# Kernel optimization log

Measured on AMD Instinct MI355X. Metric: run time of the kernel, lower is better.

## Reference

```python
import jax, jax.numpy as jnp
import numpy as np

N, M, E, HID, H = 50000, 4000, 320000, 128, 2
EPS = 1e-5  # torch BatchNorm1d eps


def _lrelu(x):
    return jnp.where(x >= 0, x, 0.2 * x)


def _bn(x, g, b):
    # BatchNorm1d in training mode: biased batch statistics over dim 0
    m = x.mean(0)
    v = ((x - m) ** 2).mean(0)
    return g * (x - m) * jax.lax.rsqrt(v + EPS) + b


def _seg_softmax(a, idx, n):
    # softmax of a[E,heads] normalized per node index idx (PyG softmax)
    mx = jax.ops.segment_max(a, idx, num_segments=n)
    e = jnp.exp(a - mx[idx])
    s = jax.ops.segment_sum(e, idx, num_segments=n)
    return e / s[idx]


def _hgconv(x, he_n, he_e, he_w, W, att, bias, heads):
    # PyG HypergraphConv(use_attention=True, concat=False)
    xl = (x @ W).reshape(N, heads, HID)                  # lin(x) -> [N,heads,C]
    # hyperedge_attr = incidence^T @ x  (matches to_dense_adj path in HGAT)
    ea = jax.ops.segment_sum(x[he_n], he_e, num_segments=M)  # [M,F]
    eal = (ea @ W).reshape(M, heads, HID)                # lin(hyperedge_attr)
    a = (jnp.concatenate([xl[he_n], eal[he_e]], axis=-1) * att[0]).sum(-1)  # [E,heads]
    a = _seg_softmax(_lrelu(a), he_n, N)
    # degree normalizations
    Dn = jax.ops.segment_sum(he_w[he_e], he_n, num_segments=N)
    Dinv = jnp.where(Dn > 0, 1.0 / Dn, 0.0)
    Bn = jax.ops.segment_sum(jnp.ones((E,), x.dtype), he_e, num_segments=M)
    Binv = jnp.where(Bn > 0, 1.0 / Bn, 0.0)
    # node -> hyperedge
    m1 = Binv[he_e][:, None, None] * xl[he_n] * a[..., None]
    eo = jax.ops.segment_sum(m1, he_e, num_segments=M)   # [M,heads,C]
    # hyperedge -> node
    m2 = Dinv[he_n][:, None, None] * eo[he_e] * a[..., None]
    out = jax.ops.segment_sum(m2, he_n, num_segments=N)  # [N,heads,C]
    return out.mean(1) + bias                            # concat=False -> head mean


def _forward(x, he_w, lin1_w, lin1_b, bn1_g, bn1_b, h1_w, h1_att, h1_b,
             bn2_g, bn2_b, h2_w, h2_att, h2_b, bn3_g, bn3_b,
             lin2_w, lin2_b, bn4_g, bn4_b, he_n, he_e):
    src = x
    x = _bn(_lrelu(x @ lin1_w + lin1_b), bn1_g, bn1_b)
    x2 = _hgconv(x, he_n, he_e, he_w, h1_w, h1_att, h1_b, H)
    x = _bn(x + x2, bn2_g, bn2_b)
    x2 = _hgconv(x, he_n, he_e, he_w, h2_w, h2_att, h2_b, 1)
    x = _bn(x + x2, bn3_g, bn3_b)
    x = _lrelu(x @ lin2_w + lin2_b)
    return _bn(src + x, bn4_g, bn4_b)


def setup_inputs() -> dict:
    key = jax.random.key(0)
    ks = jax.random.split(key, 10)
    s = 0.05
    he_n = jax.random.randint(ks[0], (E,), 0, N, dtype=jnp.int32)
    he_e = (jnp.arange(E, dtype=jnp.int32) % M)  # every hyperedge id used
    return {
        'x': jax.random.normal(ks[1], (N, 128), jnp.float32),
        'he_n': he_n, 'he_e': he_e,
        'he_w': jnp.ones((M,), jnp.float32),
        'lin1_w': jax.random.normal(ks[2], (128, HID), jnp.float32) * s,
        'lin1_b': jnp.zeros((HID,), jnp.float32),
        'bn1_g': jnp.ones((HID,), jnp.float32), 'bn1_b': jnp.zeros((HID,), jnp.float32),
        'h1_w': jax.random.normal(ks[3], (HID, H * HID), jnp.float32) * s,
        'h1_att': jax.random.normal(ks[4], (1, H, 2 * HID), jnp.float32) * s,
        'h1_b': jnp.zeros((HID,), jnp.float32),
        'bn2_g': jnp.ones((HID,), jnp.float32), 'bn2_b': jnp.zeros((HID,), jnp.float32),
        'h2_w': jax.random.normal(ks[5], (HID, HID), jnp.float32) * s,
        'h2_att': jax.random.normal(ks[6], (1, 1, 2 * HID), jnp.float32) * s,
        'h2_b': jnp.zeros((HID,), jnp.float32),
        'bn3_g': jnp.ones((HID,), jnp.float32), 'bn3_b': jnp.zeros((HID,), jnp.float32),
        'lin2_w': jax.random.normal(ks[7], (HID, 128), jnp.float32) * s,
        'lin2_b': jnp.zeros((128,), jnp.float32),
        'bn4_g': jnp.ones((128,), jnp.float32), 'bn4_b': jnp.zeros((128,), jnp.float32),
    }


def reference(x, he_n, he_e, he_w, lin1_w, lin1_b, bn1_g, bn1_b, h1_w, h1_att, h1_b,
              bn2_g, bn2_b, h2_w, h2_att, h2_b, bn3_g, bn3_b,
              lin2_w, lin2_b, bn4_g, bn4_b):
    return _forward(x, he_w, lin1_w, lin1_b, bn1_g, bn1_b, h1_w, h1_att, h1_b,
                    bn2_g, bn2_b, h2_w, h2_att, h2_b, bn3_g, bn3_b,
                    lin2_w, lin2_b, bn4_g, bn4_b, he_n, he_e)
```

## Files before the change

### kernel.cpp

```cpp
#include <hip/hip_runtime.h>
#include <math.h>

constexpr int Nn = 50000;
constexpr int Mm = 4000;
constexpr int Ee = 320000;
constexpr int KPB = Ee / Mm;
constexpr float BINV = 1.0f / (float)KPB;
constexpr float EPSf = 1e-5f;
constexpr int NBKT = 16;
constexpr int NBSCAN = 49;

__device__ __forceinline__ float lrelu_f(float x) { return x >= 0.f ? x : 0.2f * x; }

__device__ __forceinline__ float wave_sum(float v) {
#pragma unroll
    for (int o = 32; o >= 1; o >>= 1) v += __shfl_xor(v, o, 64);
    return v;
}

__device__ __forceinline__ void finalize_to_lds(const float* __restrict__ st,
                                                const float* __restrict__ g,
                                                const float* __restrict__ b,
                                                float* ABsh, int t) {
    if (t < 128) {
        double ds = 0, dq = 0;
#pragma unroll
        for (int i = 0; i < NBKT; i++) {
            ds += (double)st[i * 256 + t];
            dq += (double)st[i * 256 + 128 + t];
        }
        double mean = ds / (double)Nn;
        double var = dq / (double)Nn - mean * mean;
        float rstd = (float)(1.0 / sqrt(var + (double)EPSf));
        float A = g[t] * rstd;
        ABsh[t] = A;
        ABsh[128 + t] = b[t] - (float)mean * A;
    }
    __syncthreads();
}

__device__ void scan_body(const int* __restrict__ counts, int* __restrict__ offs,
                          int b, int t) {
    __shared__ int sdi[256];
    int pre = 0;
    for (int i = t; i < b * 1024; i += 256) pre += counts[i];
    sdi[t] = pre;
    __syncthreads();
    for (int st = 128; st >= 1; st >>= 1) {
        if (t < st) sdi[t] += sdi[t + st];
        __syncthreads();
    }
    int run0 = sdi[0];
    __syncthreads();
    int c4[4];
    int s = 0;
#pragma unroll
    for (int i = 0; i < 4; i++) {
        int n = b * 1024 + t * 4 + i;
        c4[i] = (n < Nn) ? counts[n] : 0;
        s += c4[i];
    }
    sdi[t] = s;
    __syncthreads();
    for (int off = 1; off < 256; off <<= 1) {
        int v = (t >= off) ? sdi[t - off] : 0;
        __syncthreads();
        sdi[t] += v;
        __syncthreads();
    }
    int run = sdi[t] - s + run0;
#pragma unroll
    for (int i = 0; i < 4; i++) {
        int n = b * 1024 + t * 4 + i;
        if (n < Nn) offs[n] = run;
        run += c4[i];
    }
    if (b == NBSCAN - 1 && t == 255) offs[Nn] = run0 + sdi[255];
}

template <int ROWS, bool LRELU, bool PROBN, bool RESID, bool STATS, bool PACKH2, bool SCANX>
__global__ __launch_bounds__(256) void gemmT(const float* __restrict__ A, size_t aystride,
                                             const float* __restrict__ B, int ldb,
                                             const float* __restrict__ bias, float scale,
                                             const float* __restrict__ stIn,
                                             const float* __restrict__ fing,
                                             const float* __restrict__ finb,
                                             const float* __restrict__ resid,
                                             float* __restrict__ stF,
                                             float* __restrict__ C, int ldc, int R,
                                             int gemmBlocksX,
                                             const int* __restrict__ counts,
                                             int* __restrict__ offs) {
    constexpr int RPT = ROWS / 16;
    const int t = threadIdx.x;
    if (SCANX && (int)blockIdx.x >= gemmBlocksX) {
        if (blockIdx.y == 0) scan_body(counts, offs, blockIdx.x - gemmBlocksX, t);
        return;
    }
    __shared__ float As[16][ROWS + 4];
    __shared__ float Bs[16][128];
    __shared__ float Sred[STATS ? 16 : 1][STATS ? 128 : 1];
    __shared__ float ABsh[PROBN ? 256 : 1];
    const int ty = t >> 4, tx = t & 15;
    const int row0 = blockIdx.x * ROWS;
    const int bcol = blockIdx.y * 128;
    A += (size_t)blockIdx.y * aystride;

    if (PROBN) finalize_to_lds(stIn, fing, finb, ABsh, t);

    float4 acc[RPT][2];
#pragma unroll
    for (int i = 0; i < RPT; i++)
#pragma unroll
        for (int q = 0; q < 2; q++) acc[i][q] = make_float4(0.f, 0.f, 0.f, 0.f);

    for (int k0 = 0; k0 < 128; k0 += 16) {
        {
            int r = t >> 3, kc = (t & 7) * 2;
            int rr = row0 + r;
            rr = rr < R ? rr : R - 1;
            float2 av = *(const float2*)(A + (size_t)rr * 128 + k0 + kc);
            if (PROBN) {
                av.x = av.x * ABsh[k0 + kc] + ABsh[128 + k0 + kc];
                av.y = av.y * ABsh[k0 + kc + 1] + ABsh[128 + k0 + kc + 1];
            }
            As[kc + 0][r] = av.x;
            As[kc + 1][r] = av.y;
        }
        {
            int kk = t >> 5, c4 = (t & 31) * 4;
            float4 bv0 = *(const float4*)(B + (size_t)(k0 + kk) * ldb + bcol + c4);
            float4 bv1 = *(const float4*)(B + (size_t)(k0 + kk + 8) * ldb + bcol + c4);
            *(float4*)&Bs[kk][c4] = bv0;
            *(float4*)&Bs[kk + 8][c4] = bv1;
        }
        __syncthreads();
#pragma unroll
        for (int kk = 0; kk < 16; kk++) {
            float ar[RPT];
            float2 a2 = *(const float2*)&As[kk][ty * 2];
            ar[0] = a2.x; ar[RPT - 1] = a2.y;
            float4 b0 = *(const float4*)&Bs[kk][4 * tx];
            float4 b1 = *(const float4*)&Bs[kk][64 + 4 * tx];
#pragma unroll
            for (int i = 0; i < RPT; i++) {
                acc[i][0].x = fmaf(ar[i], b0.x, acc[i][0].x);
                acc[i][0].y = fmaf(ar[i], b0.y, acc[i][0].y);
                acc[i][0].z = fmaf(ar[i], b0.z, acc[i][0].z);
                acc[i][0].w = fmaf(ar[i], b0.w, acc[i][0].w);
                acc[i][1].x = fmaf(ar[i], b1.x, acc[i][1].x);
                acc[i][1].y = fmaf(ar[i], b1.y, acc[i][1].y);
                acc[i][1].z = fmaf(ar[i], b1.z, acc[i][1].z);
                acc[i][1].w = fmaf(ar[i], b1.w, acc[i][1].w);
            }
        }
        __syncthreads();
    }

    float4 bv0 = make_float4(0.f, 0.f, 0.f, 0.f), bv1 = bv0;
    if (bias) {
        bv0 = *(const float4*)(bias + bcol + 4 * tx);
        bv1 = *(const float4*)(bias + bcol + 64 + 4 * tx);
    }
    float4 cs0 = make_float4(0.f, 0.f, 0.f, 0.f), cs1 = cs0, cq0 = cs0, cq1 = cs0;
#pragma unroll
    for (int i = 0; i < RPT; i++) {
        int row = row0 + ty * RPT + i;
        if (row >= R) continue;
        float4 v0, v1;
        v0.x = acc[i][0].x * scale + bv0.x; v0.y = acc[i][0].y * scale + bv0.y;
        v0.z = acc[i][0].z * scale + bv0.z; v0.w = acc[i][0].w * scale + bv0.w;
        v1.x = acc[i][1].x * scale + bv1.x; v1.y = acc[i][1].y * scale + bv1.y;
        v1.z = acc[i][1].z * scale + bv1.z; v1.w = acc[i][1].w * scale + bv1.w;
        if (LRELU) {
            v0.x = lrelu_f(v0.x); v0.y = lrelu_f(v0.y); v0.z = lrelu_f(v0.z); v0.w = lrelu_f(v0.w);
            v1.x = lrelu_f(v1.x); v1.y = lrelu_f(v1.y); v1.z = lrelu_f(v1.z); v1.w = lrelu_f(v1.w);
        }
        if (RESID) {
            float4 r0 = *(const float4*)(resid + (size_t)row * 128 + bcol + 4 * tx);
            float4 r1 = *(const float4*)(resid + (size_t)row * 128 + bcol + 64 + 4 * tx);
            v0.x += r0.x; v0.y += r0.y; v0.z += r0.z; v0.w += r0.w;
            v1.x += r1.x; v1.y += r1.y; v1.z += r1.z; v1.w += r1.w;
        }
        if (PACKH2) {
            int h = blockIdx.y;
            float* c0 = C + (size_t)row * ldc + 8 * tx + 2 * h;
            *(float2*)(c0) = make_float2(v0.x, v0.y);
            *(float2*)(c0 + 4) = make_float2(v0.z, v0.w);
            float* c1 = C + (size_t)row * ldc + 128 + 8 * tx + 2 * h;
            *(float2*)(c1) = make_float2(v1.x, v1.y);
            *(float2*)(c1 + 4) = make_float2(v1.z, v1.w);
        } else {
            *(float4*)(C + (size_t)row * ldc + bcol + 4 * tx) = v0;
            *(float4*)(C + (size_t)row * ldc + bcol + 64 + 4 * tx) = v1;
        }
        if (STATS) {
            cs0.x += v0.x; cs0.y += v0.y; cs0.z += v0.z; cs0.w += v0.w;
            cs1.x += v1.x; cs1.y += v1.y; cs1.z += v1.z; cs1.w += v1.w;
            cq0.x += v0.x * v0.x; cq0.y += v0.y * v0.y; cq0.z += v0.z * v0.z; cq0.w += v0.w * v0.w;
            cq1.x += v1.x * v1.x; cq1.y += v1.y * v1.y; cq1.z += v1.z * v1.z; cq1.w += v1.w * v1.w;
        }
    }
    if (STATS) {
        int bkt = blockIdx.x & (NBKT - 1);
#pragma unroll
        for (int pass = 0; pass < 2; pass++) {
            *(float4*)&Sred[ty][4 * tx] = pass ? cq0 : cs0;
            *(float4*)&Sred[ty][64 + 4 * tx] = pass ? cq1 : cs1;
            __syncthreads();
            if (t < 128) {
                float tot = 0.f;
#pragma unroll
                for (int r = 0; r < 16; r++) tot += Sred[r][t];
                atomicAdd(&stF[bkt * 256 + pass * 128 + t], tot);
            }
            __syncthreads();
        }
    }
}

__global__ void count_edges_watt(const int* __restrict__ he_n, int* __restrict__ counts,
                                 const float* __restrict__ h1_w, const float* __restrict__ h1_att,
                                 const float* __restrict__ h2_w, const float* __restrict__ h2_att,
                                 float* __restrict__ wnA, float* __restrict__ weA) {
    int t = threadIdx.x;
    if (blockIdx.x == 1250) {
        for (int j = 0; j < 3; j++) {
            int id = t + 256 * j;
            if (id >= 768) break;
            int which = id / 384;
            int rem = id % 384;
            int h3 = rem >> 7, k = rem & 127;
            float s = 0.f;
            if (h3 < 2) {
                const float* wrow = h1_w + (size_t)k * 256 + h3 * 128;
                const float* arow = h1_att + h3 * 256 + which * 128;
                for (int c = 0; c < 128; c++) s += wrow[c] * arow[c];
            } else {
                const float* wrow = h2_w + (size_t)k * 128;
                const float* arow = h2_att + which * 128;
                for (int c = 0; c < 128; c++) s += wrow[c] * arow[c];
            }
            (which ? weA : wnA)[h3 * 128 + k] = s;
        }
        return;
    }
    int e = blockIdx.x * 256 + t;
    if (e < Ee) atomicAdd(&counts[he_n[e]], 1);
}

template <int H, bool FILL>
__global__ __launch_bounds__(256) void bn_dots(const float* __restrict__ X,
                                               const float* __restrict__ stIn,
                                               const float* __restrict__ fing,
                                               const float* __restrict__ finb,
                                               float* __restrict__ ABout,
                                               const float* __restrict__ wn,
                                               const float* __restrict__ we,
                                               float* __restrict__ an,
                                               float* __restrict__ pe,
                                               const int* __restrict__ he_n,
                                               const int* __restrict__ offs,
                                               int* __restrict__ cursor,
                                               int* __restrict__ eid, int mainBlocks) {
    int t = threadIdx.x;
    if (FILL && (int)blockIdx.x >= mainBlocks) {
        int e = (blockIdx.x - mainBlocks) * 256 + t;
        if (e < Ee) {
            int n = he_n[e];
            int p = atomicAdd(&cursor[n], 1);
            eid[offs[n] + p] = e;
        }
        return;
    }
    __shared__ float ABsh[256];
    finalize_to_lds(stIn, fing, finb, ABsh, t);
    if (blockIdx.x == 0) ABout[t] = ABsh[t];
    int w = t >> 6, lane = t & 63;
    float a0 = ABsh[lane], a1 = ABsh[lane + 64];
    float b0 = ABsh[128 + lane], b1 = ABsh[192 + lane];
    float wn0[H], wn1[H], we0[H], we1[H];
#pragma unroll
    for (int h = 0; h < H; h++) {
        wn0[h] = wn[h * 128 + lane]; wn1[h] = wn[h * 128 + 64 + lane];
        we0[h] = we[h * 128 + lane]; we1[h] = we[h * 128 + 64 + lane];
    }
#pragma unroll
    for (int nn = 0; nn < 4; nn++) {
        int row = blockIdx.x * 16 + w * 4 + nn;
        const float* xr = X + (size_t)row * 128;
        float v0 = xr[lane] * a0 + b0;
        float v1 = xr[lane + 64] * a1 + b1;
        float pv[H], qv[H];
#pragma unroll
        for (int h = 0; h < H; h++) {
            pv[h] = wave_sum(v0 * wn0[h] + v1 * wn1[h]);
            qv[h] = wave_sum(v0 * we0[h] + v1 * we1[h]);
        }
        if (lane == 0) {
            if (H == 2) {
                *(float2*)&an[row * 2] = make_float2(pv[0], pv[1]);
                *(float2*)&pe[row * 2] = make_float2(qv[0], qv[1]);
            } else {
                an[row] = pv[0];
                pe[row] = qv[0];
            }
        }
    }
}

__global__ __launch_bounds__(256) void bn_out(const float* __restrict__ X,
                                              const float* __restrict__ stIn,
                                              const float* __restrict__ fing,
                                              const float* __restrict__ finb,
                                              float* __restrict__ Y) {
    __shared__ float ABsh[256];
    int t = threadIdx.x;
    finalize_to_lds(stIn, fing, finb, ABsh, t);
    int w = t >> 6, lane = t & 63;
    float a0 = ABsh[lane], a1 = ABsh[lane + 64];
    float b0 = ABsh[128 + lane], b1 = ABsh[192 + lane];
#pragma unroll
    for (int nn = 0; nn < 4; nn++) {
        int row = blockIdx.x * 16 + w * 4 + nn;
        const float* xr = X + (size_t)row * 128;
        float* yr = Y + (size_t)row * 128;
        yr[lane] = xr[lane] * a0 + b0;
        yr[lane + 64] = xr[lane + 64] * a1 + b1;
    }
}

template <int H>
__global__ __launch_bounds__(256) void ea_from_pe(const int* __restrict__ he_n,
                                                  const float* __restrict__ pe,
                                                  float* __restrict__ ae) {
    int w = threadIdx.x >> 6, lane = threadIdx.x & 63;
    int m = blockIdx.x * 4 + w;
    if (m >= Mm) return;
    float s[H];
#pragma unroll
    for (int h = 0; h < H; h++) s[h] = 0.f;
    for (int k = lane; k < KPB; k += 64) {
        int idx = he_n[m + k * Mm];
        if (H == 2) {
            float2 p2 = *(const float2*)(pe + (size_t)idx * 2);
            s[0] += p2.x;
            s[H - 1] += p2.y;
        } else {
            s[0] += pe[idx];
        }
    }
#pragma unroll
    for (int h = 0; h < H; h++) s[h] = wave_sum(s[h]);
    if (lane == 0)
#pragma unroll
        for (int h = 0; h < H; h++) ae[m * H + h] = s[h];
}

template <int H>
__global__ __launch_bounds__(256) void seg_softmax(const int* __restrict__ offs,
                                                   const int* __restrict__ eid,
                                                   const float* __restrict__ an,
                                                   const float* __restrict__ ae,
                                                   const float* __restrict__ he_w,
                                                   float* __restrict__ aw,
                                                   float* __restrict__ sdl) {
    int t = threadIdx.x;
    int wv = t >> 6, lane = t & 63;
    int q = lane >> 3, li = lane & 7;
    int n = blockIdx.x * 32 + wv * 8 + q;
    bool valid = n < Nn;
    int base = valid ? offs[n] : 0;
    int deg = valid ? offs[n + 1] - base : 0;
    float anv[H];
#pragma unroll
    for (int h = 0; h < H; h++) anv[h] = valid ? an[n * H + h] : 0.f;

    bool h0 = li < deg, h1 = li + 8 < deg;
    int e0 = 0, e1 = 0, m0 = 0, m1 = 0;
    float l0[H], l1[H];
    float mx[H];
#pragma unroll
    for (int h = 0; h < H; h++) { mx[h] = -INFINITY; l0[h] = 0.f; l1[h] = 0.f; }
    if (h0) {
        e0 = eid[base + li];
        m0 = e0 % Mm;
#pragma unroll
        for (int h = 0; h < H; h++) {
            l0[h] = lrelu_f(anv[h] + ae[m0 * H + h]);
            mx[h] = fmaxf(mx[h], l0[h]);
        }
    }
    if (h1) {
        e1 = eid[base + li + 8];
        m1 = e1 % Mm;
#pragma unroll
        for (int h = 0; h < H; h++) {
            l1[h] = lrelu_f(anv[h] + ae[m1 * H + h]);
            mx[h] = fmaxf(mx[h], l1[h]);
        }
    }
    for (int c = li + 16; c < deg; c += 8) {
        int e = eid[base + c];
        int m = e % Mm;
#pragma unroll
        for (int h = 0; h < H; h++) mx[h] = fmaxf(mx[h], lrelu_f(anv[h] + ae[m * H + h]));
    }
#pragma unroll
    for (int h = 0; h < H; h++) {
#pragma unroll
        for (int o = 1; o <= 4; o <<= 1) mx[h] = fmaxf(mx[h], __shfl_xor(mx[h], o, 64));
    }
    float sm[H], p0[H], p1[H];
#pragma unroll
    for (int h = 0; h < H; h++) { sm[h] = 0.f; p0[h] = 0.f; p1[h] = 0.f; }
    float dn = 0.f;
    if (h0) {
        dn += he_w[m0];
#pragma unroll
        for (int h = 0; h < H; h++) { p0[h] = expf(l0[h] - mx[h]); sm[h] += p0[h]; }
    }
    if (h1) {
        dn += he_w[m1];
#pragma unroll
        for (int h = 0; h < H; h++) { p1[h] = expf(l1[h] - mx[h]); sm[h] += p1[h]; }
    }
    for (int c = li + 16; c < deg; c += 8) {
        int e = eid[base + c];
        int m = e % Mm;
        dn += he_w[m];
#pragma unroll
        for (int h = 0; h < H; h++) sm[h] += expf(lrelu_f(anv[h] + ae[m * H + h]) - mx[h]);
    }
#pragma unroll
    for (int o = 1; o <= 4; o <<= 1) dn += __shfl_xor(dn, o, 64);
#pragma unroll
    for (int h = 0; h < H; h++) {
#pragma unroll
        for (int o = 1; o <= 4; o <<= 1) sm[h] += __shfl_xor(sm[h], o, 64);
    }
    float Dv = dn > 0.f ? 1.0f / dn : 0.0f;
    float premul = Dv * (H == 2 ? 0.5f : 1.0f);
    if (h0) {
        float p[H];
#pragma unroll
        for (int h = 0; h < H; h++) p[h] = p0[h] / sm[h];
        if (H == 2) {
            *(float2*)(aw + (size_t)e0 * 2) = make_float2(p[0], p[1]);
            *(float4*)(sdl + (size_t)(base + li) * 4) =
                make_float4(__int_as_float(m0), p[0] * premul, p[H - 1] * premul, 0.f);
        } else {
            aw[e0] = p[0];
            *(float2*)(sdl + (size_t)(base + li) * 2) = make_float2(__int_as_float(m0), p[0] * premul);
        }
    }
    if (h1) {
        float p[H];
#pragma unroll
        for (int h = 0; h < H; h++) p[h] = p1[h] / sm[h];
        if (H == 2) {
            *(float2*)(aw + (size_t)e1 * 2) = make_float2(p[0], p[1]);
            *(float4*)(sdl + (size_t)(base + li + 8) * 4) =
                make_float4(__int_as_float(m1), p[0] * premul, p[H - 1] * premul, 0.f);
        } else {
            aw[e1] = p[0];
            *(float2*)(sdl + (size_t)(base + li + 8) * 2) =
                make_float2(__int_as_float(m1), p[0] * premul);
        }
    }
    for (int c = li + 16; c < deg; c += 8) {
        int e = eid[base + c];
        int m = e % Mm;
        float p[H];
#pragma unroll
        for (int h = 0; h < H; h++) p[h] = expf(lrelu_f(anv[h] + ae[m * H + h]) - mx[h]) / sm[h];
        if (H == 2) {
            *(float2*)(aw + (size_t)e * 2) = make_float2(p[0], p[1]);
            *(float4*)(sdl + (size_t)(base + c) * 4) =
                make_float4(__int_as_float(m), p[0] * premul, p[H - 1] * premul, 0.f);
        } else {
            aw[e] = p[0];
            *(float2*)(sdl + (size_t)(base + c) * 2) = make_float2(__int_as_float(m), p[0] * premul);
        }
    }
}

template <int H>
__global__ __launch_bounds__(256) void s_build(const float* __restrict__ X,
                                               const float* __restrict__ AB,
                                               const int* __restrict__ he_n,
                                               const float* __restrict__ aw,
                                               float* __restrict__ S) {
    __shared__ int idx[KPB];
    __shared__ float av[KPB][H];
    __shared__ float red[8][H][128];
    int m = blockIdx.x, t = threadIdx.x;
    int g = t >> 5, l = t & 31;
    if (t < KPB) idx[t] = he_n[m + t * Mm];
    for (int q2 = t; q2 < KPB * H; q2 += 256) {
        int k = q2 / H, h = q2 - k * H;
        av[k][h] = aw[(size_t)(m + k * Mm) * H + h];
    }
    __syncthreads();
    float4 A4 = ((const float4*)AB)[l];
    float4 B4 = ((const float4*)(AB + 128))[l];
    float4 acc[H];
#pragma unroll
    for (int h = 0; h < H; h++) acc[h] = make_float4(0.f, 0.f, 0.f, 0.f);
#pragma unroll
    for (int kk = 0; kk < KPB / 8; kk++) {
        int k = g + kk * 8;
        float4 v = ((const float4*)(X + (size_t)idx[k] * 128))[l];
        v.x = v.x * A4.x + B4.x;
        v.y = v.y * A4.y + B4.y;
        v.z = v.z * A4.z + B4.z;
        v.w = v.w * A4.w + B4.w;
#pragma unroll
        for (int h = 0; h < H; h++) {
            float a = av[k][h];
            acc[h].x = fmaf(a, v.x, acc[h].x);
            acc[h].y = fmaf(a, v.y, acc[h].y);
            acc[h].z = fmaf(a, v.z, acc[h].z);
            acc[h].w = fmaf(a, v.w, acc[h].w);
        }
    }
#pragma unroll
    for (int h = 0; h < H; h++) *(float4*)&red[g][h][l * 4] = acc[h];
    __syncthreads();
    if (t < 32 * H) {
        int h = t >> 5, l2 = t & 31;
        float4 s = make_float4(0.f, 0.f, 0.f, 0.f);
#pragma unroll
        for (int gg = 0; gg < 8; gg++) {
            float4 r = *(const float4*)&red[gg][h][l2 * 4];
            s.x += r.x; s.y += r.y; s.z += r.z; s.w += r.w;
        }
        ((float4*)(S + ((size_t)h * Mm + m) * 128))[l2] = s;
    }
}

template <int H>
__global__ __launch_bounds__(256) void node_agg(const int* __restrict__ offs,
                                                const float* __restrict__ sdl,
                                                const float* __restrict__ eo,
                                                const float* __restrict__ bias,
                                                const float* __restrict__ AB,
                                                float* __restrict__ stF,
                                                float* __restrict__ T) {
    __shared__ float smem[4][256];
    __shared__ float redS[4][128], redQ[4][128];
    int t = threadIdx.x;
    int w = t >> 6, lane = t & 63;
    int n0 = blockIdx.x * 16 + w * 4;
    int o = offs[n0 + (lane < 4 ? lane : 4)];
    int b0 = __shfl(o, 0, 64);
    int b1 = __shfl(o, 1, 64);
    int b2 = __shfl(o, 2, 64);
    int b3 = __shfl(o, 3, 64);
    int b4 = __shfl(o, 4, 64);
    int cnt = b4 - b0;
    int cnt64 = cnt < 64 ? cnt : 64;

    if (lane < cnt64) {
        int slot = b0 + lane;
        if (H == 2) {
            *(float4*)&smem[w][4 * lane] = *(const float4*)(sdl + (size_t)slot * 4);
        } else {
            *(float2*)&smem[w][2 * lane] = *(const float2*)(sdl + (size_t)slot * 2);
        }
    }
    __syncthreads();

    int s1 = min(b1 - b0, cnt64), s2 = min(b2 - b0, cnt64), s3 = min(b3 - b0, cnt64);
    float2 acc0 = make_float2(0.f, 0.f), acc1 = acc0, acc2 = acc0, acc3 = acc0;

#define NA_BODY(ACC, CBEG, CEND)                                                \
    {                                                                           \
        int c = (CBEG);                                                         \
        for (; c + 1 < (CEND); c += 2) {                                        \
            if (H == 2) {                                                       \
                float4 sa = *(const float4*)&smem[w][4 * c];                    \
                float4 sb = *(const float4*)&smem[w][4 * (c + 1)];              \
                float4 ea = *(const float4*)(eo + (size_t)__float_as_int(sa.x) * 256 + 4 * lane); \
                float4 eb = *(const float4*)(eo + (size_t)__float_as_int(sb.x) * 256 + 4 * lane); \
                ACC.x += sa.y * ea.x + sa.z * ea.z + sb.y * eb.x + sb.z * eb.z; \
                ACC.y += sa.y * ea.y + sa.z * ea.w + sb.y * eb.y + sb.z * eb.w; \
            } else {                                                            \
                float2 sa = *(const float2*)&smem[w][2 * c];                    \
                float2 sb = *(const float2*)&smem[w][2 * (c + 1)];              \
                float2 ea = *(const float2*)(eo + (size_t)__float_as_int(sa.x) * 128 + 2 * lane); \
                float2 eb = *(const float2*)(eo + (size_t)__float_as_int(sb.x) * 128 + 2 * lane); \
                ACC.x += sa.y * ea.x + sb.y * eb.x;                             \
                ACC.y += sa.y * ea.y + sb.y * eb.y;                             \
            }                                                                   \
        }                                                                       \
        if (c < (CEND)) {                                                       \
            if (H == 2) {                                                       \
                float4 sa = *(const float4*)&smem[w][4 * c];                    \
                float4 ea = *(const float4*)(eo + (size_t)__float_as_int(sa.x) * 256 + 4 * lane); \
                ACC.x += sa.y * ea.x + sa.z * ea.z;                             \
                ACC.y += sa.y * ea.y + sa.z * ea.w;                             \
            } else {                                                            \
                float2 sa = *(const float2*)&smem[w][2 * c];                    \
                float2 ea = *(const float2*)(eo + (size_t)__float_as_int(sa.x) * 128 + 2 * lane); \
                ACC.x += sa.y * ea.x;                                           \
                ACC.y += sa.y * ea.y;                                           \
            }                                                                   \
        }                                                                       \
    }
    NA_BODY(acc0, 0, s1)
    NA_BODY(acc1, s1, s2)
    NA_BODY(acc2, s2, s3)
    NA_BODY(acc3, s3, cnt64)
#undef NA_BODY

    for (int ss = 64; ss < cnt; ss++) {
        int slot = b0 + ss;
        int j = (slot >= b1) + (slot >= b2) + (slot >= b3);
        float cx, cy;
        if (H == 2) {
            float4 v = *(const float4*)(sdl + (size_t)slot * 4);
            float4 ev = *(const float4*)(eo + (size_t)__float_as_int(v.x) * 256 + 4 * lane);
            cx = v.y * ev.x + v.z * ev.z;
            cy = v.y * ev.y + v.z * ev.w;
        } else {
            float2 v = *(const float2*)(sdl + (size_t)slot * 2);
            float2 ev = *(const float2*)(eo + (size_t)__float_as_int(v.x) * 128 + 2 * lane);
            cx = v.y * ev.x;
            cy = v.y * ev.y;
        }
        if (j == 0) { acc0.x += cx; acc0.y += cy; }
        else if (j == 1) { acc1.x += cx; acc1.y += cy; }
        else if (j == 2) { acc2.x += cx; acc2.y += cy; }
        else { acc3.x += cx; acc3.y += cy; }
    }

    int col = 2 * lane;
    float2 A2 = *(const float2*)(AB + col);
    float2 B2 = *(const float2*)(AB + 128 + col);
    float2 bi = *(const float2*)(bias + col);
    float cs0 = 0.f, cs1 = 0.f, cq0 = 0.f, cq1 = 0.f;
    float2 accs[4] = {acc0, acc1, acc2, acc3};
#pragma unroll
    for (int j = 0; j < 4; j++) {
        int n = n0 + j;
        float2 xr = *(const float2*)(T + (size_t)n * 128 + col);
        float r0 = xr.x * A2.x + B2.x + bi.x + accs[j].x;
        float r1 = xr.y * A2.y + B2.y + bi.y + accs[j].y;
        *(float2*)(T + (size_t)n * 128 + col) = make_float2(r0, r1);
        cs0 += r0; cs1 += r1;
        cq0 += r0 * r0; cq1 += r1 * r1;
    }
    redS[w][col] = cs0; redS[w][col + 1] = cs1;
    redQ[w][col] = cq0; redQ[w][col + 1] = cq1;
    __syncthreads();
    if (t < 128) {
        float s = 0.f, qq = 0.f;
#pragma unroll
        for (int ww = 0; ww < 4; ww++) { s += redS[ww][t]; qq += redQ[ww][t]; }
        int bkt = blockIdx.x & (NBKT - 1);
        atomicAdd(&stF[bkt * 256 + t], s);
        atomicAdd(&stF[bkt * 256 + 128 + t], qq);
    }
}

extern "C" void kernel_launch(void* const* d_in, const int* in_sizes, int n_in,
                              void* d_out, int out_size, void* d_ws, size_t ws_size,
                              hipStream_t stream) {
    const float* x = (const float*)d_in[0];
    const int* he_n = (const int*)d_in[1];
    const float* he_w = (const float*)d_in[3];
    const float* lin1_w = (const float*)d_in[4];
    const float* lin1_b = (const float*)d_in[5];
    const float* bn1_g = (const float*)d_in[6];
    const float* bn1_b = (const float*)d_in[7];
    const float* h1_w = (const float*)d_in[8];
    const float* h1_att = (const float*)d_in[9];
    const float* h1_b = (const float*)d_in[10];
    const float* bn2_g = (const float*)d_in[11];
    const float* bn2_b = (const float*)d_in[12];
    const float* h2_w = (const float*)d_in[13];
    const float* h2_att = (const float*)d_in[14];
    const float* h2_b = (const float*)d_in[15];
    const float* bn3_g = (const float*)d_in[16];
    const float* bn3_b = (const float*)d_in[17];
    const float* lin2_w = (const float*)d_in[18];
    const float* lin2_b = (const float*)d_in[19];
    const float* bn4_g = (const float*)d_in[20];
    const float* bn4_b = (const float*)d_in[21];
    float* out = (float*)d_out;

    char* ws = (char*)d_ws;
    size_t off = 0;
    auto alloc = [&](size_t bytes) -> char* {
        char* p = ws + off;
        off = (off + bytes + 255) & ~(size_t)255;
        return p;
    };
    int* counts = (int*)alloc((size_t)Nn * 4);
    int* cursor = (int*)alloc((size_t)Nn * 4);
    float* stats = (float*)alloc((size_t)4 * NBKT * 256 * 4);
    size_t zbytes = off;
    int* offs = (int*)alloc((size_t)(Nn + 1) * 4);
    int* eid = (int*)alloc((size_t)Ee * 4);
    float* an = (float*)alloc((size_t)Nn * 2 * 4);
    float* pe = (float*)alloc((size_t)Nn * 2 * 4);
    float* ae = (float*)alloc((size_t)Mm * 2 * 4);
    float* aw = (float*)alloc((size_t)Ee * 2 * 4);
    float* sdl = (float*)alloc((size_t)Ee * 4 * 4);
    float* S = (float*)alloc((size_t)2 * Mm * 128 * 4);
    float* eo = (float*)alloc((size_t)2 * Mm * 128 * 4);
    float* wnA = (float*)alloc(384 * 4);
    float* weA = (float*)alloc(384 * 4);
    float* AB = (float*)alloc(2 * 256 * 4);
    float* buf = (float*)alloc((size_t)Nn * 128 * 4);

    float* st0 = stats;
    float* st1 = stats + NBKT * 256;
    float* st2 = stats + 2 * NBKT * 256;
    float* st3 = stats + 3 * NBKT * 256;
    float *AB1 = AB, *AB2 = AB + 256;

    hipMemsetAsync(d_ws, 0, zbytes, stream);

    constexpr int GB32 = (Nn + 31) / 32;
    count_edges_watt<<<1251, 256, 0, stream>>>(he_n, counts, h1_w, h1_att, h2_w, h2_att,
                                               wnA, weA);

    gemmT<32, true, false, false, true, false, true><<<dim3(GB32 + NBSCAN, 1), 256, 0, stream>>>(
        x, 0, lin1_w, 128, lin1_b, 1.f, nullptr, nullptr, nullptr, nullptr, st0, buf, 128, Nn,
        GB32, counts, offs);
    bn_dots<2, true><<<3125 + 1250, 256, 0, stream>>>(buf, st0, bn1_g, bn1_b, AB1, wnA, weA,
                                                      an, pe, he_n, offs, cursor, eid, 3125);

    ea_from_pe<2><<<Mm / 4, 256, 0, stream>>>(he_n, pe, ae);
    seg_softmax<2><<<(Nn + 31) / 32, 256, 0, stream>>>(offs, eid, an, ae, he_w, aw, sdl);
    s_build<2><<<Mm, 256, 0, stream>>>(buf, AB1, he_n, aw, S);
    gemmT<32, false, false, false, false, true, false><<<dim3(125, 2), 256, 0, stream>>>(
        S, (size_t)Mm * 128, h1_w, 256, nullptr, BINV, nullptr, nullptr, nullptr, nullptr,
        nullptr, eo, 256, Mm, 125, nullptr, nullptr);
    node_agg<2><<<3125, 256, 0, stream>>>(offs, sdl, eo, h1_b, AB1, st1, buf);

    bn_dots<1, false><<<3125, 256, 0, stream>>>(buf, st1, bn2_g, bn2_b, AB2, wnA + 256,
                                                weA + 256, an, pe, nullptr, nullptr, nullptr,
                                                nullptr, 3125);

    ea_from_pe<1><<<Mm / 4, 256, 0, stream>>>(he_n, pe, ae);
    seg_softmax<1><<<(Nn + 31) / 32, 256, 0, stream>>>(offs, eid, an, ae, he_w, aw, sdl);
    s_build<1><<<Mm, 256, 0, stream>>>(buf, AB2, he_n, aw, S);
    gemmT<32, false, false, false, false, false, false><<<dim3(125, 1), 256, 0, stream>>>(
        S, 0, h2_w, 128, nullptr, BINV, nullptr, nullptr, nullptr, nullptr, nullptr,
        eo, 128, Mm, 125, nullptr, nullptr);
    node_agg<1><<<3125, 256, 0, stream>>>(offs, sdl, eo, h2_b, AB2, st2, buf);

    gemmT<32, true, true, true, true, false, false><<<dim3(GB32, 1), 256, 0, stream>>>(
        buf, 0, lin2_w, 128, lin2_b, 1.f, st2, bn3_g, bn3_b, x, st3, buf, 128, Nn,
        GB32, nullptr, nullptr);
    bn_out<<<3125, 256, 0, stream>>>(buf, st3, bn4_g, bn4_b, out);
}
```

Baseline: 404.5 us.

## Shift preprocessing stages one launch later to drop the separate count kernel

The edge-count and attention-weight precompute blocks now ride along with the first GEMM launch, the prefix scan moves into the first bn_dots launch, and the CSR fill moves into the first ea_from_pe launch. The standalone count kernel is removed, saving one launch and its serialization point. Each dependent stage still runs after its producer because kernels on the stream are ordered. In exchange, the extra side blocks lengthen the tail of the kernels that host them, and the preprocessing chain now spans three launches.

```diff
diff --git a/kernel.cpp b/kernel.cpp
--- a/kernel.cpp
+++ b/kernel.cpp
@@ -9,6 +9,8 @@
 constexpr float EPSf = 1e-5f;
 constexpr int NBKT = 16;
 constexpr int NBSCAN = 49;
+constexpr int NBFILL = 1250;
+constexpr int NBCNT = 1251;
 
 __device__ __forceinline__ float lrelu_f(float x) { return x >= 0.f ? x : 0.2f * x; }
 
@@ -78,7 +80,30 @@
     if (b == NBSCAN - 1 && t == 255) offs[Nn] = run0 + sdi[255];
 }
 
-template <int ROWS, bool LRELU, bool PROBN, bool RESID, bool STATS, bool PACKH2, bool SCANX>
+__device__ void watt_body(const float* __restrict__ h1_w, const float* __restrict__ h1_att,
+                          const float* __restrict__ h2_w, const float* __restrict__ h2_att,
+                          float* __restrict__ wnA, float* __restrict__ weA, int t) {
+    for (int j = 0; j < 3; j++) {
+        int id = t + 256 * j;
+        if (id >= 768) break;
+        int which = id / 384;
+        int rem = id % 384;
+        int h3 = rem >> 7, k = rem & 127;
+        float s = 0.f;
+        if (h3 < 2) {
+            const float* wrow = h1_w + (size_t)k * 256 + h3 * 128;
+            const float* arow = h1_att + h3 * 256 + which * 128;
+            for (int c = 0; c < 128; c++) s += wrow[c] * arow[c];
+        } else {
+            const float* wrow = h2_w + (size_t)k * 128;
+            const float* arow = h2_att + which * 128;
+            for (int c = 0; c < 128; c++) s += wrow[c] * arow[c];
+        }
+        (which ? weA : wnA)[h3 * 128 + k] = s;
+    }
+}
+
+template <int ROWS, bool LRELU, bool PROBN, bool RESID, bool STATS, bool PACKH2, bool CNTW>
 __global__ __launch_bounds__(256) void gemmT(const float* __restrict__ A, size_t aystride,
                                              const float* __restrict__ B, int ldb,
                                              const float* __restrict__ bias, float scale,
@@ -89,12 +114,24 @@
                                              float* __restrict__ stF,
                                              float* __restrict__ C, int ldc, int R,
                                              int gemmBlocksX,
-                                             const int* __restrict__ counts,
-                                             int* __restrict__ offs) {
+                                             const int* __restrict__ he_n,
+                                             int* __restrict__ counts,
+                                             const float* __restrict__ h1_w,
+                                             const float* __restrict__ h1_att,
+                                             const float* __restrict__ h2_w,
+                                             const float* __restrict__ h2_att,
+                                             float* __restrict__ wnA,
+                                             float* __restrict__ weA) {
     constexpr int RPT = ROWS / 16;
     const int t = threadIdx.x;
-    if (SCANX && (int)blockIdx.x >= gemmBlocksX) {
-        if (blockIdx.y == 0) scan_body(counts, offs, blockIdx.x - gemmBlocksX, t);
+    if (CNTW && (int)blockIdx.x >= gemmBlocksX) {
+        int cb = blockIdx.x - gemmBlocksX;
+        if (cb < NBCNT - 1) {
+            int e = cb * 256 + t;
+            if (e < Ee) atomicAdd(&counts[he_n[e]], 1);
+        } else {
+            watt_body(h1_w, h1_att, h2_w, h2_att, wnA, weA, t);
+        }
         return;
     }
     __shared__ float As[16][ROWS + 4];
@@ -219,37 +256,7 @@
     }
 }
 
-__global__ void count_edges_watt(const int* __restrict__ he_n, int* __restrict__ counts,
-                                 const float* __restrict__ h1_w, const float* __restrict__ h1_att,
-                                 const float* __restrict__ h2_w, const float* __restrict__ h2_att,
-                                 float* __restrict__ wnA, float* __restrict__ weA) {
-    int t = threadIdx.x;
-    if (blockIdx.x == 1250) {
-        for (int j = 0; j < 3; j++) {
-            int id = t + 256 * j;
-            if (id >= 768) break;
-            int which = id / 384;
-            int rem = id % 384;
-            int h3 = rem >> 7, k = rem & 127;
-            float s = 0.f;
-            if (h3 < 2) {
-                const float* wrow = h1_w + (size_t)k * 256 + h3 * 128;
-                const float* arow = h1_att + h3 * 256 + which * 128;
-                for (int c = 0; c < 128; c++) s += wrow[c] * arow[c];
-            } else {
-                const float* wrow = h2_w + (size_t)k * 128;
-                const float* arow = h2_att + which * 128;
-                for (int c = 0; c < 128; c++) s += wrow[c] * arow[c];
-            }
-            (which ? weA : wnA)[h3 * 128 + k] = s;
-        }
-        return;
-    }
-    int e = blockIdx.x * 256 + t;
-    if (e < Ee) atomicAdd(&counts[he_n[e]], 1);
-}
-
-template <int H, bool FILL>
+template <int H, bool SCAN>
 __global__ __launch_bounds__(256) void bn_dots(const float* __restrict__ X,
                                                const float* __restrict__ stIn,
                                                const float* __restrict__ fing,
@@ -259,18 +266,11 @@
                                                const float* __restrict__ we,
                                                float* __restrict__ an,
                                                float* __restrict__ pe,
-                                               const int* __restrict__ he_n,
-                                               const int* __restrict__ offs,
-                                               int* __restrict__ cursor,
-                                               int* __restrict__ eid, int mainBlocks) {
+                                               const int* __restrict__ counts,
+                                               int* __restrict__ offs, int mainBlocks) {
     int t = threadIdx.x;
-    if (FILL && (int)blockIdx.x >= mainBlocks) {
-        int e = (blockIdx.x - mainBlocks) * 256 + t;
-        if (e < Ee) {
-            int n = he_n[e];
-            int p = atomicAdd(&cursor[n], 1);
-            eid[offs[n] + p] = e;
-        }
+    if (SCAN && (int)blockIdx.x >= mainBlocks) {
+        scan_body(counts, offs, blockIdx.x - mainBlocks, t);
         return;
     }
     __shared__ float ABsh[256];
@@ -330,11 +330,24 @@
     }
 }
 
-template <int H>
+template <int H, bool FILL>
 __global__ __launch_bounds__(256) void ea_from_pe(const int* __restrict__ he_n,
                                                   const float* __restrict__ pe,
-                                                  float* __restrict__ ae) {
-    int w = threadIdx.x >> 6, lane = threadIdx.x & 63;
+                                                  float* __restrict__ ae,
+                                                  const int* __restrict__ offs,
+                                                  int* __restrict__ cursor,
+                                                  int* __restrict__ eid, int mainBlocks) {
+    int t = threadIdx.x;
+    if (FILL && (int)blockIdx.x >= mainBlocks) {
+        int e = (blockIdx.x - mainBlocks) * 256 + t;
+        if (e < Ee) {
+            int n = he_n[e];
+            int p = atomicAdd(&cursor[n], 1);
+            eid[offs[n] + p] = e;
+        }
+        return;
+    }
+    int w = t >> 6, lane = t & 63;
     int m = blockIdx.x * 4 + w;
     if (m >= Mm) return;
     float s[H];
@@ -724,37 +737,38 @@
     hipMemsetAsync(d_ws, 0, zbytes, stream);
 
     constexpr int GB32 = (Nn + 31) / 32;
-    count_edges_watt<<<1251, 256, 0, stream>>>(he_n, counts, h1_w, h1_att, h2_w, h2_att,
-                                               wnA, weA);
-
-    gemmT<32, true, false, false, true, false, true><<<dim3(GB32 + NBSCAN, 1), 256, 0, stream>>>(
+
+    gemmT<32, true, false, false, true, false, true><<<dim3(GB32 + NBCNT, 1), 256, 0, stream>>>(
         x, 0, lin1_w, 128, lin1_b, 1.f, nullptr, nullptr, nullptr, nullptr, st0, buf, 128, Nn,
-        GB32, counts, offs);
-    bn_dots<2, true><<<3125 + 1250, 256, 0, stream>>>(buf, st0, bn1_g, bn1_b, AB1, wnA, weA,
-                                                      an, pe, he_n, offs, cursor, eid, 3125);
-
-    ea_from_pe<2><<<Mm / 4, 256, 0, stream>>>(he_n, pe, ae);
+        GB32, he_n, counts, h1_w, h1_att, h2_w, h2_att, wnA, weA);
+    bn_dots<2, true><<<3125 + NBSCAN, 256, 0, stream>>>(buf, st0, bn1_g, bn1_b, AB1, wnA, weA,
+                                                        an, pe, counts, offs, 3125);
+
+    ea_from_pe<2, true><<<Mm / 4 + NBFILL, 256, 0, stream>>>(he_n, pe, ae, offs, cursor, eid,
+                                                             Mm / 4);
     seg_softmax<2><<<(Nn + 31) / 32, 256, 0, stream>>>(offs, eid, an, ae, he_w, aw, sdl);
     s_build<2><<<Mm, 256, 0, stream>>>(buf, AB1, he_n, aw, S);
     gemmT<32, false, false, false, false, true, false><<<dim3(125, 2), 256, 0, stream>>>(
         S, (size_t)Mm * 128, h1_w, 256, nullptr, BINV, nullptr, nullptr, nullptr, nullptr,
-        nullptr, eo, 256, Mm, 125, nullptr, nullptr);
+        nullptr, eo, 256, Mm, 125, nullptr, nullptr, nullptr, nullptr, nullptr, nullptr,
+        nullptr, nullptr);
     node_agg<2><<<3125, 256, 0, stream>>>(offs, sdl, eo, h1_b, AB1, st1, buf);
 
     bn_dots<1, false><<<3125, 256, 0, stream>>>(buf, st1, bn2_g, bn2_b, AB2, wnA + 256,
-                                                weA + 256, an, pe, nullptr, nullptr, nullptr,
-                                                nullptr, 3125);
-
-    ea_from_pe<1><<<Mm / 4, 256, 0, stream>>>(he_n, pe, ae);
+                                                weA + 256, an, pe, nullptr, nullptr, 3125);
+
+    ea_from_pe<1, false><<<Mm / 4, 256, 0, stream>>>(he_n, pe, ae, nullptr, nullptr, nullptr,
+                                                     Mm / 4);
     seg_softmax<1><<<(Nn + 31) / 32, 256, 0, stream>>>(offs, eid, an, ae, he_w, aw, sdl);
     s_build<1><<<Mm, 256, 0, stream>>>(buf, AB2, he_n, aw, S);
     gemmT<32, false, false, false, false, false, false><<<dim3(125, 1), 256, 0, stream>>>(
         S, 0, h2_w, 128, nullptr, BINV, nullptr, nullptr, nullptr, nullptr, nullptr,
-        eo, 128, Mm, 125, nullptr, nullptr);
+        eo, 128, Mm, 125, nullptr, nullptr, nullptr, nullptr, nullptr, nullptr,
+        nullptr, nullptr);
     node_agg<1><<<3125, 256, 0, stream>>>(offs, sdl, eo, h2_b, AB2, st2, buf);
 
     gemmT<32, true, true, true, true, false, false><<<dim3(GB32, 1), 256, 0, stream>>>(
         buf, 0, lin2_w, 128, lin2_b, 1.f, st2, bn3_g, bn3_b, x, st3, buf, 128, Nn,
-        GB32, nullptr, nullptr);
+        GB32, nullptr, nullptr, nullptr, nullptr, nullptr, nullptr, nullptr, nullptr);
     bn_out<<<3125, 256, 0, stream>>>(buf, st3, bn4_g, bn4_b, out);
 }
```

Result: no change. 400.8 us (-0.9%).
